# Kernel optimization log

Measured on AMD Instinct MI355X. Metric: run time of the kernel, lower is better.

## Reference

```python
import jax, jax.numpy as jnp
import numpy as np

B, S, D, H = 2, 2048, 1024, 16
HD = D // H  # head_dim = 64

def setup_inputs() -> dict:
    key = jax.random.key(0)
    ks = jax.random.split(key, 12)
    sc = 0.02
    return {
        "x": jax.random.normal(ks[0], (B, S, D), dtype=jnp.float32),
        "docking_scores": jax.random.uniform(ks[1], (B, S), dtype=jnp.float32),
        # weights stored as (in, out): y = x @ W + b (equivalent to torch Linear with W=weight.T)
        "Wq": jax.random.normal(ks[2], (D, D), dtype=jnp.float32) * sc,
        "bq": jnp.zeros((D,), dtype=jnp.float32),
        "Wk": jax.random.normal(ks[3], (D, D), dtype=jnp.float32) * sc,
        "bk": jnp.zeros((D,), dtype=jnp.float32),
        "Wv": jax.random.normal(ks[4], (D, D), dtype=jnp.float32) * sc,
        "bv": jnp.zeros((D,), dtype=jnp.float32),
        "Wo": jax.random.normal(ks[5], (D, D), dtype=jnp.float32) * sc,
        "bo": jnp.zeros((D,), dtype=jnp.float32),
        "beta": jnp.asarray(0.5, dtype=jnp.float32),
    }

def reference(x, docking_scores, Wq, bq, Wk, bk, Wv, bv, Wo, bo, beta):
    b, s, d = x.shape
    # project and split heads: (B, H, S, HD)
    def heads(y):
        return y.reshape(b, s, H, HD).transpose(0, 2, 1, 3)
    Q = heads(x @ Wq + bq)
    K = heads(x @ Wk + bk)
    V = heads(x @ Wv + bv)
    # full attention scores (B, H, S, S) — materialized as in the source
    scores = jnp.einsum('bhqd,bhkd->bhqk', Q, K) / np.float32(np.sqrt(HD))
    attn = jax.nn.softmax(scores, axis=-1)
    # docking blend: daa_type != ALL -> blend with per-key docking scores
    ds = docking_scores[:, None, None, :]  # (B, 1, 1, S)
    attn = (1.0 - beta) * attn + beta * ds
    ctx = jnp.einsum('bhqk,bhkd->bhqd', attn, V)
    ctx = ctx.transpose(0, 2, 1, 3).reshape(b, s, d)
    return ctx @ Wo + bo
```

## Files before the change

### kernel.cpp

```cpp
#include <hip/hip_runtime.h>

typedef __attribute__((ext_vector_type(8))) short short8;
typedef __attribute__((ext_vector_type(4))) short short4v;
typedef __attribute__((ext_vector_type(4))) float f32x4;

#if __has_builtin(__builtin_amdgcn_exp2f)
#define EXP2F(x) __builtin_amdgcn_exp2f(x)
#define QSCALE 0.1803368801111601f
#else
#define EXP2F(x) __expf(x)
#define QSCALE 0.125f
#endif

__device__ __forceinline__ short f2bf(float f) {
  unsigned u = __builtin_bit_cast(unsigned, f);
  u += 0x7fffu + ((u >> 16) & 1u);
  return (short)(u >> 16);
}
__device__ __forceinline__ float bf2f(short s) {
  unsigned u = ((unsigned)(unsigned short)s) << 16;
  return __builtin_bit_cast(float, u);
}
__device__ __forceinline__ void async_load16(const short* g, short* l) {
  __builtin_amdgcn_global_load_lds(
      (const __attribute__((address_space(1))) unsigned int*)g,
      (__attribute__((address_space(3))) unsigned int*)l, 16, 0, 0);
}

__global__ __launch_bounds__(256) void convert_x(const float* __restrict__ x,
                                                 short* __restrict__ xb) {
  int i = (blockIdx.x * 256 + threadIdx.x) * 4;
  float4 v = *(const float4*)(x + i);
  short4v o;
  o[0] = f2bf(v.x); o[1] = f2bf(v.y); o[2] = f2bf(v.z); o[3] = f2bf(v.w);
  *(short4v*)(xb + i) = o;
}

__global__ __launch_bounds__(256) void transpose_w(
    const float* __restrict__ W0, const float* __restrict__ W1,
    const float* __restrict__ W2, const float* __restrict__ W3,
    short* __restrict__ T0, short* __restrict__ T1,
    short* __restrict__ T2, short* __restrict__ T3) {
  const float* W; short* T;
  switch (blockIdx.z) {
    case 0: W = W0; T = T0; break;
    case 1: W = W1; T = T1; break;
    case 2: W = W2; T = T2; break;
    default: W = W3; T = T3; break;
  }
  __shared__ float tile[32][33];
  int tx = threadIdx.x & 31, ty = threadIdx.x >> 5;
  int c = blockIdx.x * 32 + tx;
  #pragma unroll
  for (int i = 0; i < 4; ++i) {
    int r = blockIdx.y * 32 + ty + i * 8;
    tile[ty + i * 8][tx] = W[(size_t)r * 1024 + c];
  }
  __syncthreads();
  int k = blockIdx.y * 32 + tx;
  #pragma unroll
  for (int i = 0; i < 4; ++i) {
    int n = blockIdx.x * 32 + ty + i * 8;
    T[(size_t)n * 1024 + k] = f2bf(tile[tx][ty + i * 8]);
  }
}

__device__ __forceinline__ void gemm_core_128(
    const short* __restrict__ A, const short* __restrict__ Bt,
    int m0, int n0, short* As, short* Bs, f32x4 acc[4][4]) {
  const int tid = threadIdx.x;
  const int wave = tid >> 6, lane = tid & 63;
  const int wm = wave >> 1, wn = wave & 1;
  const int lr = lane & 15, quad = lane >> 4;
  for (int k0 = 0; k0 < 1024; k0 += 32) {
    __syncthreads();
    #pragma unroll
    for (int c2 = 0; c2 < 2; ++c2) {
      int c = wave * 2 + c2;
      int row = c * 16 + (lane >> 2);
      int cbp = lane & 3;
      int sw = (cbp ^ ((row >> 1) & 3)) << 3;
      async_load16(A + (size_t)(m0 + row) * 1024 + k0 + sw, As + c * 512);
      async_load16(Bt + (size_t)(n0 + row) * 1024 + k0 + sw, Bs + c * 512);
    }
    __syncthreads();
    short8 af[4], bfr[4];
    #pragma unroll
    for (int i = 0; i < 4; ++i) {
      int ra = wm * 64 + i * 16 + lr;
      af[i] = *(const short8*)(As + ra * 32 + ((quad ^ ((ra >> 1) & 3)) << 3));
      int rb = wn * 64 + i * 16 + lr;
      bfr[i] = *(const short8*)(Bs + rb * 32 + ((quad ^ ((rb >> 1) & 3)) << 3));
    }
    #pragma unroll
    for (int i = 0; i < 4; ++i)
      #pragma unroll
      for (int j = 0; j < 4; ++j)
        acc[i][j] = __builtin_amdgcn_mfma_f32_16x16x32_bf16(af[i], bfr[j], acc[i][j], 0, 0, 0);
  }
}

__global__ __launch_bounds__(256, 2) void qkv_gemm(
    const short* __restrict__ xb,
    const short* __restrict__ WqT, const short* __restrict__ WkT, const short* __restrict__ WvT,
    const float* __restrict__ bq, const float* __restrict__ bk, const float* __restrict__ bv,
    short* __restrict__ Qb, short* __restrict__ Kb, short* __restrict__ Vt) {
  __shared__ short As[128 * 32];
  __shared__ short Bs[128 * 32];
  int which = blockIdx.x >> 3;
  int n0 = (blockIdx.x & 7) * 128;
  int m0 = blockIdx.y * 128;
  const short* Bt = (which == 0) ? WqT : (which == 1) ? WkT : WvT;
  const float* bias = (which == 0) ? bq : (which == 1) ? bk : bv;
  f32x4 acc[4][4] = {};
  gemm_core_128(xb, Bt, m0, n0, As, Bs, acc);
  const int lane = threadIdx.x & 63, wave = threadIdx.x >> 6;
  const int wm = wave >> 1, wn = wave & 1;
  const int lr = lane & 15, quad = lane >> 4;
  if (which < 2) {
    short* Out = (which == 0) ? Qb : Kb;
    const float scale = (which == 0) ? QSCALE : 1.0f;
    #pragma unroll
    for (int i = 0; i < 4; ++i)
      #pragma unroll
      for (int j = 0; j < 4; ++j) {
        int col = n0 + wn * 64 + j * 16 + lr;
        float bb = bias[col];
        int rowb = m0 + wm * 64 + i * 16 + quad * 4;
        #pragma unroll
        for (int r = 0; r < 4; ++r)
          Out[(size_t)(rowb + r) * 1024 + col] = f2bf((acc[i][j][r] + bb) * scale);
      }
  } else {
    #pragma unroll
    for (int i = 0; i < 4; ++i)
      #pragma unroll
      for (int j = 0; j < 4; ++j) {
        int col = n0 + wn * 64 + j * 16 + lr;
        float bb = bias[col];
        int h = col >> 6, d = col & 63;
        int rowb = m0 + wm * 64 + i * 16 + quad * 4;
        int b = rowb >> 11, s = rowb & 2047;
        short4v pk;
        #pragma unroll
        for (int r = 0; r < 4; ++r) pk[r] = f2bf(acc[i][j][r] + bb);
        *(short4v*)(Vt + ((size_t)(b * 16 + h) * 64 + d) * 2048 + s) = pk;
      }
  }
}

__global__ __launch_bounds__(256) void dsv_kernel(const short* __restrict__ Vt,
                                                  const float* __restrict__ ds,
                                                  float* __restrict__ dsV) {
  int bh = blockIdx.x, sc = blockIdx.y;
  int b = bh >> 4;
  int d = threadIdx.x >> 2, part = threadIdx.x & 3;
  const short* vrow = Vt + ((size_t)bh * 64 + d) * 2048 + sc * 256 + part * 64;
  const float* dsrow = ds + (size_t)b * 2048 + sc * 256 + part * 64;
  float acc = 0.f;
  #pragma unroll
  for (int i = 0; i < 64; i += 8) {
    short8 v = *(const short8*)(vrow + i);
    float4 f0 = *(const float4*)(dsrow + i);
    float4 f1 = *(const float4*)(dsrow + i + 4);
    acc += f0.x * bf2f(v[0]) + f0.y * bf2f(v[1]) + f0.z * bf2f(v[2]) + f0.w * bf2f(v[3]);
    acc += f1.x * bf2f(v[4]) + f1.y * bf2f(v[5]) + f1.z * bf2f(v[6]) + f1.w * bf2f(v[7]);
  }
  acc += __shfl_xor(acc, 1);
  acc += __shfl_xor(acc, 2);
  if (part == 0) atomicAdd(dsV + bh * 64 + d, acc);
}

__global__ __launch_bounds__(256, 2) void attn_kernel(
    const short* __restrict__ Qb, const short* __restrict__ Kb,
    const short* __restrict__ Vt, const float* __restrict__ dsV,
    const float* __restrict__ beta_p, short* __restrict__ ctx) {
  __shared__ short smem[32768];
  const int tid = threadIdx.x, wave = tid >> 6, lane = tid & 63;
  const int bh = blockIdx.x >> 4, qt = blockIdx.x & 15;
  const int b = bh >> 4, h = bh & 15;
  const size_t bS = (size_t)b * 2048;
  const int lr = lane & 15, quad = lane >> 4;
  const int qg = wave & 1, half = wave >> 1;
  const int q0 = qt * 128 + qg * 64;
  const int lm7 = lane & 7;
  const int l7 = lr & 7;

  short* Ksh = smem + half * 8192;
  short* Vsh = Ksh + 4096;
  short* myP = smem + 16384 + wave * 4096;

  short8 qf[4][2];
  #pragma unroll
  for (int mb = 0; mb < 4; ++mb)
    #pragma unroll
    for (int c = 0; c < 2; ++c)
      qf[mb][c] = *(const short8*)(Qb + (bS + q0 + mb * 16 + lr) * 1024 + h * 64 + c * 32 + quad * 8);

  f32x4 O[4][4] = {};
  float lacc[4] = {0.f, 0.f, 0.f, 0.f};

  const int srow = lane >> 3;
  const int scb = (lane & 7) ^ srow;

  for (int t = 0; t < 16; ++t) {
    const int k0 = (half * 16 + t) * 64;
    __syncthreads();
    if (qg == 0) {
      #pragma unroll
      for (int c = 0; c < 8; ++c) {
        int rk = c * 8 + srow;
        async_load16(Kb + (bS + k0 + rk) * 1024 + h * 64 + scb * 8, Ksh + c * 512);
      }
    } else {
      #pragma unroll
      for (int c = 0; c < 8; ++c) {
        int rv = c * 8 + srow;
        async_load16(Vt + ((size_t)bh * 64 + rv) * 2048 + k0 + scb * 8, Vsh + c * 512);
      }
    }
    __syncthreads();

    #pragma unroll
    for (int kb = 0; kb < 4; ++kb) {
      const short* kr = Ksh + (kb * 16 + lr) * 64;
      short8 kf0 = *(const short8*)(kr + ((quad ^ l7) << 3));
      short8 kf1 = *(const short8*)(kr + (((4 + quad) ^ l7) << 3));
      #pragma unroll
      for (int mb = 0; mb < 4; ++mb) {
        f32x4 st = {0.f, 0.f, 0.f, 0.f};
        st = __builtin_amdgcn_mfma_f32_16x16x32_bf16(kf0, qf[mb][0], st, 0, 0, 0);
        st = __builtin_amdgcn_mfma_f32_16x16x32_bf16(kf1, qf[mb][1], st, 0, 0, 0);
        float p0 = EXP2F(st[0]), p1 = EXP2F(st[1]);
        float p2 = EXP2F(st[2]), p3 = EXP2F(st[3]);
        lacc[mb] += (p0 + p1) + (p2 + p3);
        unsigned a0 = __builtin_bit_cast(unsigned, p0) + 0x8000u;
        unsigned a1 = __builtin_bit_cast(unsigned, p1) + 0x8000u;
        unsigned a2 = __builtin_bit_cast(unsigned, p2) + 0x8000u;
        unsigned a3 = __builtin_bit_cast(unsigned, p3) + 0x8000u;
        uint2 pk;
        pk.x = __builtin_amdgcn_perm(a1, a0, 0x07060302u);
        pk.y = __builtin_amdgcn_perm(a3, a2, 0x07060302u);
        int phys = (4 * kb + quad) ^ (2 * l7);
        *(uint2*)(myP + (mb * 16 + lr) * 64 + phys * 4) = pk;
      }
    }
    #pragma unroll
    for (int kc = 0; kc < 2; ++kc) {
      short8 pf[4];
      #pragma unroll
      for (int mb = 0; mb < 4; ++mb) {
        int phys = (8 * kc + 2 * quad) ^ (2 * l7);
        pf[mb] = *(const short8*)(myP + (mb * 16 + lr) * 64 + phys * 4);
      }
      #pragma unroll
      for (int db = 0; db < 4; ++db) {
        const short* vr = Vsh + (db * 16 + lr) * 64;
        short8 vf = *(const short8*)(vr + (((kc * 4 + quad) ^ l7) << 3));
        #pragma unroll
        for (int mb = 0; mb < 4; ++mb)
          O[mb][db] = __builtin_amdgcn_mfma_f32_16x16x32_bf16(vf, pf[mb], O[mb][db], 0, 0, 0);
      }
    }
  }

  float* Obuf = (float*)smem;
  float* lbuf = (float*)(smem + 16384);
  const int qs = (quad + lr) & 3;
  __syncthreads();
  if (half == 1) {
    #pragma unroll
    for (int mb = 0; mb < 4; ++mb) {
      #pragma unroll
      for (int db = 0; db < 4; ++db)
        *(f32x4*)(Obuf + ((qg * 4 + mb) * 4 + db) * 256 + lr * 16 + qs * 4) = O[mb][db];
      lbuf[(qg * 4 + mb) * 64 + quad * 16 + lr] = lacc[mb];
    }
  }
  __syncthreads();
  if (half == 0) {
    float beta = *beta_p;
    #pragma unroll
    for (int mb = 0; mb < 4; ++mb) {
      #pragma unroll
      for (int db = 0; db < 4; ++db)
        O[mb][db] += *(const f32x4*)(Obuf + ((qg * 4 + mb) * 4 + db) * 256 + lr * 16 + qs * 4);
      float v = lacc[mb] + lbuf[(qg * 4 + mb) * 64 + quad * 16 + lr];
      v += __shfl_xor(v, 16);
      v += __shfl_xor(v, 32);
      float linv = (1.f - beta) / v;
      #pragma unroll
      for (int db = 0; db < 4; ++db) {
        float4 dv = *(const float4*)(dsV + bh * 64 + db * 16 + quad * 4);
        short4v o;
        o[0] = f2bf(O[mb][db][0] * linv + beta * dv.x);
        o[1] = f2bf(O[mb][db][1] * linv + beta * dv.y);
        o[2] = f2bf(O[mb][db][2] * linv + beta * dv.z);
        o[3] = f2bf(O[mb][db][3] * linv + beta * dv.w);
        *(short4v*)(ctx + (bS + q0 + mb * 16 + lr) * 1024 + h * 64 + db * 16 + quad * 4) = o;
      }
    }
  }
}

__global__ __launch_bounds__(256, 2) void out_gemm(
    const short* __restrict__ ctx, const short* __restrict__ WoT,
    const float* __restrict__ bo, float* __restrict__ out) {
  __shared__ short As[64 * 32];
  __shared__ short Bs[128 * 32];
  const int n0 = blockIdx.x * 128, m0 = blockIdx.y * 64;
  const int tid = threadIdx.x, wave = tid >> 6, lane = tid & 63;
  const int wm = wave >> 1, wn = wave & 1;
  const int lr = lane & 15, quad = lane >> 4;
  f32x4 acc[2][4] = {};
  for (int k0 = 0; k0 < 1024; k0 += 32) {
    __syncthreads();
    #pragma unroll
    for (int c3 = 0; c3 < 3; ++c3) {
      int idx = wave * 3 + c3;
      int rloc = lane >> 2;
      int cbp = lane & 3;
      if (idx < 4) {
        int row = idx * 16 + rloc;
        int sw = (cbp ^ ((row >> 1) & 3)) << 3;
        async_load16(ctx + (size_t)(m0 + row) * 1024 + k0 + sw, As + idx * 512);
      } else {
        int c = idx - 4;
        int row = c * 16 + rloc;
        int sw = (cbp ^ ((row >> 1) & 3)) << 3;
        async_load16(WoT + (size_t)(n0 + row) * 1024 + k0 + sw, Bs + c * 512);
      }
    }
    __syncthreads();
    short8 af[2], bfr[4];
    #pragma unroll
    for (int i = 0; i < 2; ++i) {
      int ra = wm * 32 + i * 16 + lr;
      af[i] = *(const short8*)(As + ra * 32 + ((quad ^ ((ra >> 1) & 3)) << 3));
    }
    #pragma unroll
    for (int j = 0; j < 4; ++j) {
      int rb = wn * 64 + j * 16 + lr;
      bfr[j] = *(const short8*)(Bs + rb * 32 + ((quad ^ ((rb >> 1) & 3)) << 3));
    }
    #pragma unroll
    for (int i = 0; i < 2; ++i)
      #pragma unroll
      for (int j = 0; j < 4; ++j)
        acc[i][j] = __builtin_amdgcn_mfma_f32_16x16x32_bf16(af[i], bfr[j], acc[i][j], 0, 0, 0);
  }
  #pragma unroll
  for (int i = 0; i < 2; ++i)
    #pragma unroll
    for (int j = 0; j < 4; ++j) {
      int col = n0 + wn * 64 + j * 16 + lr;
      float bb = bo[col];
      int rowb = m0 + wm * 32 + i * 16 + quad * 4;
      #pragma unroll
      for (int r = 0; r < 4; ++r)
        out[(size_t)(rowb + r) * 1024 + col] = acc[i][j][r] + bb;
    }
}

extern "C" void kernel_launch(void* const* d_in, const int* in_sizes, int n_in,
                              void* d_out, int out_size, void* d_ws, size_t ws_size,
                              hipStream_t stream) {
  const float* x    = (const float*)d_in[0];
  const float* dsc  = (const float*)d_in[1];
  const float* Wq   = (const float*)d_in[2];
  const float* bq   = (const float*)d_in[3];
  const float* Wk   = (const float*)d_in[4];
  const float* bk   = (const float*)d_in[5];
  const float* Wv   = (const float*)d_in[6];
  const float* bv   = (const float*)d_in[7];
  const float* Wo   = (const float*)d_in[8];
  const float* bo   = (const float*)d_in[9];
  const float* beta = (const float*)d_in[10];

  char* ws = (char*)d_ws;
  const size_t MB = 1u << 20;
  short* xb  = (short*)(ws + 0 * MB);
  short* WqT = (short*)(ws + 8 * MB);
  short* WkT = (short*)(ws + 10 * MB);
  short* WvT = (short*)(ws + 12 * MB);
  short* WoT = (short*)(ws + 14 * MB);
  short* Qb  = (short*)(ws + 16 * MB);
  short* Kb  = (short*)(ws + 24 * MB);
  short* Vt  = (short*)(ws + 32 * MB);
  float* dsV = (float*)(ws + 40 * MB);
  short* ctx = xb;

  convert_x<<<4096, 256, 0, stream>>>(x, xb);
  transpose_w<<<dim3(32, 32, 4), 256, 0, stream>>>(Wq, Wk, Wv, Wo, WqT, WkT, WvT, WoT);
  qkv_gemm<<<dim3(24, 32), 256, 0, stream>>>(xb, WqT, WkT, WvT, bq, bk, bv, Qb, Kb, Vt);
  hipMemsetAsync(dsV, 0, 32 * 64 * sizeof(float), stream);
  dsv_kernel<<<dim3(32, 8), 256, 0, stream>>>(Vt, dsc, dsV);
  attn_kernel<<<512, 256, 0, stream>>>(Qb, Kb, Vt, dsV, beta, ctx);
  out_gemm<<<dim3(8, 64), 256, 0, stream>>>(ctx, WoT, bo, (float*)d_out);
}
```

Before: 205.4 us.

## Load K/V fragments directly from global memory, drop split-K halves in attention

The attention kernel no longer stages K and V tiles in shared memory with async loads and barriers. Each of two waves now loads its MFMA K and V fragments straight from global memory and walks the full key range, so the cross-wave reduction of partial O and row sums at the end goes away. Blocks shrink to 128 threads and use far less LDS, which should allow more resident blocks. In exchange, K and V are read redundantly per wave through L2/L1 with strided, less coalesced accesses, and there is less memory-latency hiding per wave.

```diff
diff --git a/kernel.cpp b/kernel.cpp
--- a/kernel.cpp
+++ b/kernel.cpp
@@ -171,24 +171,22 @@
   if (part == 0) atomicAdd(dsV + bh * 64 + d, acc);
 }
 
-__global__ __launch_bounds__(256, 2) void attn_kernel(
+__global__ __launch_bounds__(128, 3) void attn_kernel(
     const short* __restrict__ Qb, const short* __restrict__ Kb,
     const short* __restrict__ Vt, const float* __restrict__ dsV,
     const float* __restrict__ beta_p, short* __restrict__ ctx) {
-  __shared__ short smem[32768];
+  __shared__ short Pbuf[2][4096];
   const int tid = threadIdx.x, wave = tid >> 6, lane = tid & 63;
   const int bh = blockIdx.x >> 4, qt = blockIdx.x & 15;
   const int b = bh >> 4, h = bh & 15;
   const size_t bS = (size_t)b * 2048;
   const int lr = lane & 15, quad = lane >> 4;
-  const int qg = wave & 1, half = wave >> 1;
-  const int q0 = qt * 128 + qg * 64;
-  const int lm7 = lane & 7;
+  const int q0 = qt * 128 + wave * 64;
   const int l7 = lr & 7;
 
-  short* Ksh = smem + half * 8192;
-  short* Vsh = Ksh + 4096;
-  short* myP = smem + 16384 + wave * 4096;
+  short* myP = Pbuf[wave];
+  const short* Kbase = Kb + bS * 1024 + h * 64 + quad * 8;
+  const short* Vbase = Vt + (size_t)bh * 64 * 2048 + quad * 8;
 
   short8 qf[4][2];
   #pragma unroll
@@ -200,32 +198,13 @@
   f32x4 O[4][4] = {};
   float lacc[4] = {0.f, 0.f, 0.f, 0.f};
 
-  const int srow = lane >> 3;
-  const int scb = (lane & 7) ^ srow;
-
-  for (int t = 0; t < 16; ++t) {
-    const int k0 = (half * 16 + t) * 64;
-    __syncthreads();
-    if (qg == 0) {
-      #pragma unroll
-      for (int c = 0; c < 8; ++c) {
-        int rk = c * 8 + srow;
-        async_load16(Kb + (bS + k0 + rk) * 1024 + h * 64 + scb * 8, Ksh + c * 512);
-      }
-    } else {
-      #pragma unroll
-      for (int c = 0; c < 8; ++c) {
-        int rv = c * 8 + srow;
-        async_load16(Vt + ((size_t)bh * 64 + rv) * 2048 + k0 + scb * 8, Vsh + c * 512);
-      }
-    }
-    __syncthreads();
-
+  for (int t = 0; t < 32; ++t) {
+    const int k0 = t * 64;
     #pragma unroll
     for (int kb = 0; kb < 4; ++kb) {
-      const short* kr = Ksh + (kb * 16 + lr) * 64;
-      short8 kf0 = *(const short8*)(kr + ((quad ^ l7) << 3));
-      short8 kf1 = *(const short8*)(kr + (((4 + quad) ^ l7) << 3));
+      const short* kr = Kbase + (size_t)(k0 + kb * 16 + lr) * 1024;
+      short8 kf0 = *(const short8*)(kr);
+      short8 kf1 = *(const short8*)(kr + 32);
       #pragma unroll
       for (int mb = 0; mb < 4; ++mb) {
         f32x4 st = {0.f, 0.f, 0.f, 0.f};
@@ -255,8 +234,7 @@
       }
       #pragma unroll
       for (int db = 0; db < 4; ++db) {
-        const short* vr = Vsh + (db * 16 + lr) * 64;
-        short8 vf = *(const short8*)(vr + (((kc * 4 + quad) ^ l7) << 3));
+        short8 vf = *(const short8*)(Vbase + (size_t)(db * 16 + lr) * 2048 + k0 + kc * 32);
         #pragma unroll
         for (int mb = 0; mb < 4; ++mb)
           O[mb][db] = __builtin_amdgcn_mfma_f32_16x16x32_bf16(vf, pf[mb], O[mb][db], 0, 0, 0);
@@ -264,41 +242,22 @@
     }
   }
 
-  float* Obuf = (float*)smem;
-  float* lbuf = (float*)(smem + 16384);
-  const int qs = (quad + lr) & 3;
-  __syncthreads();
-  if (half == 1) {
-    #pragma unroll
-    for (int mb = 0; mb < 4; ++mb) {
-      #pragma unroll
-      for (int db = 0; db < 4; ++db)
-        *(f32x4*)(Obuf + ((qg * 4 + mb) * 4 + db) * 256 + lr * 16 + qs * 4) = O[mb][db];
-      lbuf[(qg * 4 + mb) * 64 + quad * 16 + lr] = lacc[mb];
-    }
-  }
-  __syncthreads();
-  if (half == 0) {
-    float beta = *beta_p;
-    #pragma unroll
-    for (int mb = 0; mb < 4; ++mb) {
-      #pragma unroll
-      for (int db = 0; db < 4; ++db)
-        O[mb][db] += *(const f32x4*)(Obuf + ((qg * 4 + mb) * 4 + db) * 256 + lr * 16 + qs * 4);
-      float v = lacc[mb] + lbuf[(qg * 4 + mb) * 64 + quad * 16 + lr];
-      v += __shfl_xor(v, 16);
-      v += __shfl_xor(v, 32);
-      float linv = (1.f - beta) / v;
-      #pragma unroll
-      for (int db = 0; db < 4; ++db) {
-        float4 dv = *(const float4*)(dsV + bh * 64 + db * 16 + quad * 4);
-        short4v o;
-        o[0] = f2bf(O[mb][db][0] * linv + beta * dv.x);
-        o[1] = f2bf(O[mb][db][1] * linv + beta * dv.y);
-        o[2] = f2bf(O[mb][db][2] * linv + beta * dv.z);
-        o[3] = f2bf(O[mb][db][3] * linv + beta * dv.w);
-        *(short4v*)(ctx + (bS + q0 + mb * 16 + lr) * 1024 + h * 64 + db * 16 + quad * 4) = o;
-      }
+  float beta = *beta_p;
+  #pragma unroll
+  for (int mb = 0; mb < 4; ++mb) {
+    float v = lacc[mb];
+    v += __shfl_xor(v, 16);
+    v += __shfl_xor(v, 32);
+    float linv = (1.f - beta) / v;
+    #pragma unroll
+    for (int db = 0; db < 4; ++db) {
+      float4 dv = *(const float4*)(dsV + bh * 64 + db * 16 + quad * 4);
+      short4v o;
+      o[0] = f2bf(O[mb][db][0] * linv + beta * dv.x);
+      o[1] = f2bf(O[mb][db][1] * linv + beta * dv.y);
+      o[2] = f2bf(O[mb][db][2] * linv + beta * dv.z);
+      o[3] = f2bf(O[mb][db][3] * linv + beta * dv.w);
+      *(short4v*)(ctx + (bS + q0 + mb * 16 + lr) * 1024 + h * 64 + db * 16 + quad * 4) = o;
     }
   }
 }
@@ -395,6 +354,6 @@
   qkv_gemm<<<dim3(24, 32), 256, 0, stream>>>(xb, WqT, WkT, WvT, bq, bk, bv, Qb, Kb, Vt);
   hipMemsetAsync(dsV, 0, 32 * 64 * sizeof(float), stream);
   dsv_kernel<<<dim3(32, 8), 256, 0, stream>>>(Vt, dsc, dsV);
-  attn_kernel<<<512, 256, 0, stream>>>(Qb, Kb, Vt, dsV, beta, ctx);
+  attn_kernel<<<512, 128, 0, stream>>>(Qb, Kb, Vt, dsV, beta, ctx);
   out_gemm<<<dim3(8, 64), 256, 0, stream>>>(ctx, WoT, bo, (float*)d_out);
 }
```

Result: slower. 314.5 us (+53.1%).
